# Optimization experiments

Hardware: AMD Instinct MI355X
Metric: run time of the kernel (lower is better)

The kernel has to match this reference:

```python
import jax, jax.numpy as jnp
import numpy as np

B, S, D, H, E = 2, 1024, 1024, 4096, 8


def _xavier(key, shape):
    # matches torch.nn.init.xavier_uniform_ on a 3D tensor: fan_in/out from last two dims
    fan_in, fan_out = shape[-2], shape[-1]
    limit = float(np.sqrt(6.0 / (fan_in + fan_out)))
    return jax.random.uniform(key, shape, jnp.float32, -limit, limit)


def setup_inputs() -> dict:
    key = jax.random.key(0)
    ks = jax.random.split(key, 4)
    x = jax.random.normal(ks[0], (B, S, D), jnp.float32)
    router_w = jax.random.normal(ks[1], (D, E), jnp.float32) * (1.0 / np.sqrt(D))
    router_b = jnp.zeros((E,), jnp.float32)
    fc1_weight = _xavier(ks[2], (E, D, H))
    fc1_bias = jnp.zeros((E, H), jnp.float32)
    fc2_weight = _xavier(ks[3], (E, H, D))
    fc2_bias = jnp.zeros((E, D), jnp.float32)
    return {
        "x": x,
        "router_w": router_w,
        "router_b": router_b,
        "fc1_weight": fc1_weight,
        "fc1_bias": fc1_bias,
        "fc2_weight": fc2_weight,
        "fc2_bias": fc2_bias,
    }


def reference(x, router_w, router_b, fc1_weight, fc1_bias, fc2_weight, fc2_bias):
    b, s, d = x.shape
    x_flat = x.reshape(-1, d)                                  # [T, D]
    logits = x_flat @ router_w + router_b                       # [T, E]
    probs = jax.nn.softmax(logits, axis=-1)                     # [T, E]
    # per-expert FC1 + exact GELU (torch nn.GELU default is erf-based)
    h = jnp.einsum('td,edh->teh', x_flat, fc1_weight) + fc1_bias  # [T, E, H]
    h = jax.nn.gelu(h, approximate=False)
    expert_out = jnp.einsum('teh,ehd->ted', h, fc2_weight) + fc2_bias  # [T, E, D]
    out_flat = jnp.einsum('te,ted->td', probs, expert_out)      # [T, D]
    y = out_flat.reshape(b, s, d)
    router_probs = probs.reshape(b, s, -1)
    return y, router_probs
```

## Files before the change

kernel.cpp:

```cpp
#include <hip/hip_runtime.h>
#include <math.h>


typedef float f32x4 __attribute__((ext_vector_type(4)));
typedef __bf16 bf16x8 __attribute__((ext_vector_type(8)));

#define GLL16(gp, lp)                                                          \
  __builtin_amdgcn_global_load_lds(                                            \
      (const __attribute__((address_space(1))) void*)(gp),                     \
      (__attribute__((address_space(3))) void*)(lp), 16, 0, 0)

__device__ __forceinline__ float gelu_f(float h) {
  float x = h * 0.70710678118654752f;
  float ax = fabsf(x);
  float t = __builtin_amdgcn_rcpf(fmaf(0.3275911f, ax, 1.0f));
  float p = fmaf(1.061405429f, t, -1.453152027f);
  p = fmaf(p, t, 1.421413741f);
  p = fmaf(p, t, -0.284496736f);
  p = fmaf(p, t, 0.254829592f);
  float e = __expf(-x * x);
  float erfv = fmaf(-p * t, e, 1.0f);
  erfv = copysignf(erfv, x);
  return 0.5f * h * (1.0f + erfv);
}

__global__ void pre_kernel(const float* __restrict__ x,
                           const float* __restrict__ rw,
                           const float* __restrict__ rb,
                           const float* __restrict__ b2,
                           float* __restrict__ PT,
                           float* __restrict__ probs_out,
                           __bf16* __restrict__ xb,
                           float* __restrict__ y)
{
  __shared__ float ps[4][8];
  const int tid = threadIdx.x;
  const int g = tid >> 6, l = tid & 63;
  const int t = blockIdx.x * 4 + g;
  const int d0 = l * 16;
  const float* xr = x + (size_t)t * 1024 + d0;

  f32x4 xv[4];
#pragma unroll
  for (int i = 0; i < 4; ++i) xv[i] = *(const f32x4*)(xr + i * 4);

  {
    bf16x8 o0, o1;
#pragma unroll
    for (int j = 0; j < 8; ++j) {
      o0[j] = (__bf16)xv[j >> 2][j & 3];
      o1[j] = (__bf16)xv[2 + (j >> 2)][j & 3];
    }
    *(bf16x8*)(xb + (size_t)t * 1024 + d0) = o0;
    *(bf16x8*)(xb + (size_t)t * 1024 + d0 + 8) = o1;
  }

  float a[8];
#pragma unroll
  for (int e = 0; e < 8; ++e) a[e] = 0.f;
#pragma unroll
  for (int i = 0; i < 16; ++i) {
    float xs = xv[i >> 2][i & 3];
    const float* wr = rw + (size_t)(d0 + i) * 8;
    f32x4 w0 = *(const f32x4*)(wr);
    f32x4 w1 = *(const f32x4*)(wr + 4);
#pragma unroll
    for (int e = 0; e < 4; ++e) a[e] = fmaf(xs, w0[e], a[e]);
#pragma unroll
    for (int e = 0; e < 4; ++e) a[4 + e] = fmaf(xs, w1[e], a[4 + e]);
  }
#pragma unroll
  for (int off = 32; off > 0; off >>= 1) {
#pragma unroll
    for (int e = 0; e < 8; ++e) a[e] += __shfl_down(a[e], off);
  }
  if (l == 0) {
#pragma unroll
    for (int e = 0; e < 8; ++e) a[e] += rb[e];
    float m = a[0];
#pragma unroll
    for (int e = 1; e < 8; ++e) m = fmaxf(m, a[e]);
    float s = 0.f;
#pragma unroll
    for (int e = 0; e < 8; ++e) { a[e] = __expf(a[e] - m); s += a[e]; }
    float inv = 1.f / s;
#pragma unroll
    for (int e = 0; e < 8; ++e) {
      float p = a[e] * inv;
      PT[(size_t)e * 2048 + t] = p;
      probs_out[t * 8 + e] = p;
      ps[g][e] = p;
    }
  }
  __syncthreads();

  f32x4 acc[4];
#pragma unroll
  for (int i = 0; i < 4; ++i) acc[i] = {0.f, 0.f, 0.f, 0.f};
#pragma unroll
  for (int e = 0; e < 8; ++e) {
    float p = ps[g][e];
#pragma unroll
    for (int i = 0; i < 4; ++i) {
      f32x4 b = *(const f32x4*)(b2 + (size_t)e * 1024 + d0 + i * 4);
#pragma unroll
      for (int c = 0; c < 4; ++c) acc[i][c] = fmaf(p, b[c], acc[i][c]);
    }
  }
#pragma unroll
  for (int i = 0; i < 4; ++i)
    *(f32x4*)(y + (size_t)t * 1024 + d0 + i * 4) = acc[i];
}

__global__ void router_kernel(const float* __restrict__ x,
                              const float* __restrict__ rw,
                              const float* __restrict__ rb,
                              float* __restrict__ probs_out)
{
  int gid = blockIdx.x * blockDim.x + threadIdx.x;
  int t = gid >> 6;
  int l = gid & 63;
  const float* xr = x + (size_t)t * 1024;
  float a[8];
#pragma unroll
  for (int e = 0; e < 8; ++e) a[e] = 0.f;
  for (int d = l; d < 1024; d += 64) {
    float xv = xr[d];
    f32x4 w0 = *(const f32x4*)(rw + d * 8);
    f32x4 w1 = *(const f32x4*)(rw + d * 8 + 4);
#pragma unroll
    for (int e = 0; e < 4; ++e) a[e] += xv * w0[e];
#pragma unroll
    for (int e = 0; e < 4; ++e) a[4 + e] += xv * w1[e];
  }
#pragma unroll
  for (int off = 32; off > 0; off >>= 1) {
#pragma unroll
    for (int e = 0; e < 8; ++e) a[e] += __shfl_down(a[e], off);
  }
  if (l == 0) {
#pragma unroll
    for (int e = 0; e < 8; ++e) a[e] += rb[e];
    float m = a[0];
#pragma unroll
    for (int e = 1; e < 8; ++e) m = fmaxf(m, a[e]);
    float s = 0.f;
#pragma unroll
    for (int e = 0; e < 8; ++e) { a[e] = __expf(a[e] - m); s += a[e]; }
    float inv = 1.f / s;
#pragma unroll
    for (int e = 0; e < 8; ++e) probs_out[t * 8 + e] = a[e] * inv;
  }
}

__global__ void transconv_kernel(const float* __restrict__ src,
                                 __bf16* __restrict__ dst,
                                 int R, int C, size_t dstLd, size_t zOff)
{
  __shared__ __bf16 tile[64][257];
  size_t bs = (size_t)blockIdx.z * (size_t)R * (size_t)C;
  size_t dzo = (size_t)blockIdx.z * zOff;
  int r0 = blockIdx.x * 64, c0 = blockIdx.y * 256;
  const int l15 = (threadIdx.x & 15) * 4;
  const int rq = threadIdx.x >> 4;
#pragma unroll
  for (int i = 0; i < 4; ++i) {
    const int row = rq + 16 * i;
    const float* sr = src + bs + (size_t)(r0 + row) * C + c0 + l15;
#pragma unroll
    for (int q = 0; q < 4; ++q) {
      f32x4 v = *(const f32x4*)(sr + q * 64);
#pragma unroll
      for (int j = 0; j < 4; ++j)
        tile[row][q * 64 + l15 + j] = (__bf16)v[j];
    }
  }
  __syncthreads();
  const int cb = threadIdx.x >> 3;
  const int orr = (threadIdx.x & 7) * 8;
#pragma unroll
  for (int g = 0; g < 8; ++g) {
    const int c = cb + 32 * g;
    bf16x8 o;
#pragma unroll
    for (int j = 0; j < 8; ++j) o[j] = tile[orr + j][c];
    *(bf16x8*)(dst + (size_t)(c0 + c) * dstLd + dzo + r0 + orr) = o;
  }
}

__device__ __forceinline__ void mfma_loop256(
    const char* Ab, const char* Bb, size_t ldaB, size_t ldbB, int K,
    char* lds, f32x4 acc[8][4])
{
  const int tid = threadIdx.x;
  const int w = tid >> 6, l = tid & 63;
  const int wm = w >> 2, wn = w & 3;
  const int m16 = l & 15, q = l >> 4;
  const int swz = m16 & 7;
  const int aBase = wm * 16384 + m16 * 128;
  const int bBase = 32768 + (wn >> 1) * 16384 + ((wn & 1) * 64 + m16) * 128;
  const int srcCh = ((l & 7) ^ ((l >> 3) & 7)) << 4;
  const size_t gA0 = (size_t)(w * 16 + (l >> 3)) * ldaB + srcCh;
  const size_t gB0 = (size_t)(w * 16 + (l >> 3)) * ldbB + srcCh;
  const int dstW = w * 2048;
  const int NT = K >> 6;

  bf16x8 af[4][2], bv[4][2];

#define STG_A(h, tau)                                                          \
  {                                                                            \
    char* d = lds + (((tau) & 1) * 65536) + (h) * 16384 + dstW;                \
    const char* g = Ab + gA0 + (size_t)((h) * 128) * ldaB + (size_t)(tau) * 128;\
    GLL16(g, d);                                                               \
    GLL16(g + 8 * ldaB, d + 1024);                                             \
  }
#define STG_B(h, tau)                                                          \
  {                                                                            \
    char* d = lds + (((tau) & 1) * 65536) + 32768 + (h) * 16384 + dstW;        \
    const char* g = Bb + gB0 + (size_t)((h) * 128) * ldbB + (size_t)(tau) * 128;\
    GLL16(g, d);                                                               \
    GLL16(g + 8 * ldbB, d + 1024);                                             \
  }
#define RD_A(lo, p)                                                            \
  _Pragma("unroll") for (int mi = 0; mi < 4; ++mi)                             \
  _Pragma("unroll") for (int ks = 0; ks < 2; ++ks)                             \
    af[mi][ks] = *(const bf16x8*)(lds + (p) * 65536 + aBase +                  \
        ((lo) * 4 + mi) * 2048 + (((ks * 4 + q) ^ swz) << 4));
#define RD_B(no, p)                                                            \
  _Pragma("unroll") for (int nj = 0; nj < 2; ++nj)                             \
  _Pragma("unroll") for (int ks = 0; ks < 2; ++ks)                             \
    bv[(no) * 2 + nj][ks] = *(const bf16x8*)(lds + (p) * 65536 + bBase +       \
        ((no) * 2 + nj) * 2048 + (((ks * 4 + q) ^ swz) << 4));
#define MM(lo, no)                                                             \
  __builtin_amdgcn_s_setprio(1);                                               \
  _Pragma("unroll") for (int mi = 0; mi < 4; ++mi)                             \
  _Pragma("unroll") for (int nj = 0; nj < 2; ++nj)                             \
  _Pragma("unroll") for (int ks = 0; ks < 2; ++ks)                             \
    acc[(lo) * 4 + mi][(no) * 2 + nj] =                                        \
        __builtin_amdgcn_mfma_f32_16x16x32_bf16(                               \
            af[mi][ks], bv[(no) * 2 + nj][ks],                                 \
            acc[(lo) * 4 + mi][(no) * 2 + nj], 0, 0, 0);                       \
  __builtin_amdgcn_s_setprio(0);
#define SB __builtin_amdgcn_sched_barrier(0)
#define BAR { SB; __builtin_amdgcn_s_barrier(); SB; }
#define VMW(n) asm volatile("s_waitcnt vmcnt(" #n ")" ::: "memory")

  STG_A(0, 0); STG_A(1, 0); STG_B(0, 0); STG_B(1, 0);
  STG_B(0, 1); STG_B(1, 1);
  VMW(4);
  BAR;

  int t = 0;
  for (; t < NT - 2; ++t) {
    const int p = t & 1;
    RD_A(0, p); RD_B(0, p);
    STG_A(0, t + 1);
    BAR; MM(0, 0); BAR;
    RD_B(1, p);
    STG_A(1, t + 1);
    BAR; MM(0, 1); BAR;
    RD_A(1, p);
    STG_B(0, t + 2);
    BAR; MM(1, 0); BAR;
    STG_B(1, t + 2);
    BAR; MM(1, 1); SB; VMW(4); BAR;
  }
  {
    const int p = t & 1;
    RD_A(0, p); RD_B(0, p);
    STG_A(0, t + 1);
    BAR; MM(0, 0); BAR;
    RD_B(1, p);
    STG_A(1, t + 1);
    BAR; MM(0, 1); BAR;
    RD_A(1, p);
    BAR; MM(1, 0); BAR;
    BAR; MM(1, 1); SB; VMW(0); BAR;
    ++t;
  }
  {
    const int p = t & 1;
    RD_A(0, p); RD_B(0, p);
    MM(0, 0);
    RD_B(1, p);
    MM(0, 1);
    RD_A(1, p);
    MM(1, 0);
    MM(1, 1);
  }
#undef STG_A
#undef STG_B
#undef RD_A
#undef RD_B
#undef MM
#undef SB
#undef BAR
#undef VMW
}

__device__ __forceinline__ int xcd_swz(int id, int nwg) {
  return ((nwg & 7) == 0) ? ((id & 7) * (nwg >> 3) + (id >> 3)) : id;
}

__global__ __launch_bounds__(512, 2) void gemm1_kernel(
    const __bf16* __restrict__ X, const __bf16* __restrict__ W1T,
    const float* __restrict__ b1, const float* __restrict__ PT,
    __bf16* __restrict__ Hs, int hs_ld, int e_off, size_t b_zstride)
{
  __shared__ __align__(16) char lds[131072];
  const int nwg = gridDim.x * gridDim.y * gridDim.z;
  const int id = blockIdx.x + gridDim.x * (blockIdx.y + gridDim.y * blockIdx.z);
  const int wg = xcd_swz(id, nwg);
  const int bm = wg & 7;
  const int bn = (wg >> 3) % gridDim.y;
  const int z = wg / (gridDim.y << 3);
  const int e = z + e_off;

  f32x4 acc[8][4];
  const f32x4 z4 = {0.f, 0.f, 0.f, 0.f};
#pragma unroll
  for (int i = 0; i < 8; ++i)
#pragma unroll
    for (int j = 0; j < 4; ++j) acc[i][j] = z4;

  const char* A = (const char*)(X + (size_t)bm * 256 * 1024);
  const char* B = (const char*)(W1T + (size_t)z * b_zstride +
                                (size_t)bn * 256 * 1024);
  mfma_loop256(A, B, 2048, 2048, 1024, lds, acc);

  const int tid = threadIdx.x, w = tid >> 6, l = tid & 63;
  const int wm = w >> 2, wn = w & 3, q = l >> 4, m16 = l & 15;
  const int row0 = bm * 256 + wm * 128 + q * 4;
  const int colE = bn * 256 + wn * 64 + m16;
  const int zcol = (hs_ld == 4096) ? 0 : z * 4096;
  float b1v[4];
#pragma unroll
  for (int nj = 0; nj < 4; ++nj)
    b1v[nj] = b1[(size_t)e * 4096 + colE + nj * 16];
#pragma unroll
  for (int mi = 0; mi < 8; ++mi) {
    float pv[4];
#pragma unroll
    for (int r = 0; r < 4; ++r)
      pv[r] = PT[(size_t)e * 2048 + row0 + mi * 16 + r];
#pragma unroll
    for (int nj = 0; nj < 4; ++nj)
#pragma unroll
      for (int r = 0; r < 4; ++r) {
        float h = acc[mi][nj][r] + b1v[nj];
        float o = gelu_f(h) * pv[r];
        Hs[(size_t)(row0 + mi * 16 + r) * hs_ld + zcol + colE + nj * 16] =
            (__bf16)o;
      }
  }
}

__global__ __launch_bounds__(512, 2) void gemm2_kernel(
    const __bf16* __restrict__ Hs, const __bf16* __restrict__ W2T,
    float* __restrict__ y, int lda, int ldb, int kz, int Kb)
{
  __shared__ __align__(16) char lds[131072];
  const int nwg = gridDim.x * gridDim.y * gridDim.z;
  const int id = blockIdx.x + gridDim.x * (blockIdx.y + gridDim.y * blockIdx.z);
  const int wg = xcd_swz(id, nwg);
  const int bm = wg & 7;
  const int bn = (wg >> 3) % gridDim.y;
  const int z = wg / (gridDim.y << 3);

  f32x4 acc[8][4];
  const f32x4 z4 = {0.f, 0.f, 0.f, 0.f};
#pragma unroll
  for (int i = 0; i < 8; ++i)
#pragma unroll
    for (int j = 0; j < 4; ++j) acc[i][j] = z4;

  const char* A = (const char*)(Hs + (size_t)bm * 256 * lda + (size_t)z * kz);
  const char* B = (const char*)(W2T + (size_t)bn * 256 * ldb + (size_t)z * kz);
  mfma_loop256(A, B, (size_t)lda * 2, (size_t)ldb * 2, Kb, lds, acc);

  const int tid = threadIdx.x, w = tid >> 6, l = tid & 63;
  const int wm = w >> 2, wn = w & 3, q = l >> 4, m16 = l & 15;
  const int row0 = bm * 256 + wm * 128 + q * 4;
  const int col0 = bn * 256 + wn * 64 + m16;
#pragma unroll
  for (int mi = 0; mi < 8; ++mi)
#pragma unroll
    for (int nj = 0; nj < 4; ++nj)
#pragma unroll
      for (int r = 0; r < 4; ++r)
        unsafeAtomicAdd(
            y + (size_t)(row0 + mi * 16 + r) * 1024 + col0 + nj * 16,
            acc[mi][nj][r]);
}

__global__ __launch_bounds__(256) void fused_naive_kernel(
    const float* __restrict__ x, const float* __restrict__ w1,
    const float* __restrict__ b1, const float* __restrict__ w2,
    const float* __restrict__ b2, const float* __restrict__ probs,
    float* __restrict__ y)
{
  __shared__ float xs[8][1024];
  __shared__ float gs[8][64];
  __shared__ float ps[8];
  const int tid = threadIdx.x;
  const int t0 = blockIdx.x * 8;
  const size_t DH = (size_t)1024 * 4096;
  const int tt = tid >> 5;
  const int d0 = (tid & 31) * 32;
  float acc[32];
#pragma unroll
  for (int i = 0; i < 32; ++i) acc[i] = 0.f;
  {
    const f32x4* xsrc = (const f32x4*)(x + (size_t)t0 * 1024);
    f32x4* xdst = (f32x4*)&xs[0][0];
    for (int i = tid; i < 2048; i += 256) xdst[i] = xsrc[i];
  }
  const int wv = tid >> 6;
  const int hl = tid & 63;
  for (int e = 0; e < 8; ++e) {
    if (tid < 8) ps[tid] = probs[(size_t)(t0 + tid) * 8 + e];
    __syncthreads();
    for (int hc = 0; hc < 4096; hc += 64) {
      float a0 = 0.f, a1 = 0.f;
      const float* w1p = w1 + (size_t)e * DH + hc + hl;
      for (int d = 0; d < 1024; ++d) {
        float wvv = w1p[(size_t)d * 4096];
        a0 += xs[wv * 2 + 0][d] * wvv;
        a1 += xs[wv * 2 + 1][d] * wvv;
      }
      __syncthreads();
      gs[wv * 2 + 0][hl] =
          ps[wv * 2 + 0] * gelu_f(a0 + b1[(size_t)e * 4096 + hc + hl]);
      gs[wv * 2 + 1][hl] =
          ps[wv * 2 + 1] * gelu_f(a1 + b1[(size_t)e * 4096 + hc + hl]);
      __syncthreads();
      const float* w2p = w2 + (size_t)e * DH + (size_t)hc * 1024 + d0;
      for (int hh = 0; hh < 64; ++hh) {
        float g = gs[tt][hh];
#pragma unroll
        for (int jb = 0; jb < 8; ++jb) {
          f32x4 w4 = *(const f32x4*)(w2p + (size_t)hh * 1024 + jb * 4);
#pragma unroll
          for (int j2 = 0; j2 < 4; ++j2) acc[jb * 4 + j2] += g * w4[j2];
        }
      }
    }
#pragma unroll
    for (int j = 0; j < 32; ++j)
      acc[j] += ps[tt] * b2[(size_t)e * 1024 + d0 + j];
    __syncthreads();
  }
  float* yp = y + (size_t)(t0 + tt) * 1024 + d0;
#pragma unroll
  for (int jb = 0; jb < 8; ++jb) {
    f32x4 o = {acc[jb * 4], acc[jb * 4 + 1], acc[jb * 4 + 2], acc[jb * 4 + 3]};
    *(f32x4*)(yp + jb * 4) = o;
  }
}

extern "C" void kernel_launch(void* const* d_in, const int* in_sizes, int n_in,
                              void* d_out, int out_size, void* d_ws,
                              size_t ws_size, hipStream_t stream)
{
  const float* x  = (const float*)d_in[0];
  const float* rw = (const float*)d_in[1];
  const float* rb = (const float*)d_in[2];
  const float* w1 = (const float*)d_in[3];
  const float* b1 = (const float*)d_in[4];
  const float* w2 = (const float*)d_in[5];
  const float* b2 = (const float*)d_in[6];
  float* y = (float*)d_out;
  float* probs_out = y + (size_t)2048 * 1024;

  const size_t DH = (size_t)1024 * 4096;
  const size_t BASE = (64 << 10) + (size_t)2048 * 1024 * 2;
  const size_t TA = BASE + 8 * DH * 2 + (size_t)2048 * 32768 * 2;
  const size_t TB = BASE + DH * 2 + (size_t)2048 * 4096 * 2;

  char* ws = (char*)d_ws;
  float* PT = (float*)ws;
  __bf16* xb = (__bf16*)(ws + (64 << 10));
  __bf16* WT = (__bf16*)(ws + BASE);

  if (ws_size >= TA) {
    pre_kernel<<<512, 256, 0, stream>>>(x, rw, rb, b2, PT, probs_out, xb, y);
    __bf16* Hs = WT + 8 * DH;
    transconv_kernel<<<dim3(16, 16, 8), 256, 0, stream>>>(
        w1, WT, 1024, 4096, 1024, DH);
    gemm1_kernel<<<dim3(8, 16, 8), 512, 0, stream>>>(xb, WT, b1, PT, Hs,
                                                     32768, 0, DH);
    transconv_kernel<<<dim3(64, 4, 8), 256, 0, stream>>>(
        w2, WT, 4096, 1024, 32768, 4096);
    gemm2_kernel<<<dim3(8, 4, 8), 512, 0, stream>>>(Hs, WT, y, 32768,
                                                    32768, 4096, 4096);
  } else if (ws_size >= TB) {
    pre_kernel<<<512, 256, 0, stream>>>(x, rw, rb, b2, PT, probs_out, xb, y);
    __bf16* HsE = WT + DH;
    for (int e = 0; e < 8; ++e) {
      transconv_kernel<<<dim3(16, 16, 1), 256, 0, stream>>>(
          w1 + (size_t)e * DH, WT, 1024, 4096, 1024, 0);
      gemm1_kernel<<<dim3(8, 16, 1), 512, 0, stream>>>(xb, WT, b1, PT, HsE,
                                                       4096, e, 0);
      transconv_kernel<<<dim3(64, 4, 1), 256, 0, stream>>>(
          w2 + (size_t)e * DH, WT, 4096, 1024, 4096, 0);
      gemm2_kernel<<<dim3(8, 4, 4), 512, 0, stream>>>(HsE, WT, y, 4096,
                                                      4096, 1024, 1024);
    }
  } else {
    router_kernel<<<512, 256, 0, stream>>>(x, rw, rb, probs_out);
    fused_naive_kernel<<<256, 256, 0, stream>>>(x, w1, b1, w2, b2, probs_out,
                                                y);
  }
}
```

Measured before the change: 607.6 us.

## Restructure MFMA main loop into two half-phases with fewer barriers

Reorganizes the double-buffered bf16 MFMA K-loop so each tile iteration issues all B and half of A LDS reads up front, runs two larger MFMA groups, and uses two workgroup barriers instead of eight. Sched_barrier fences are removed so the compiler can interleave LDS reads, global-to-LDS loads and MFMAs more freely, and the setprio window now spans a whole half-tile. The transpose-convert kernel is split into two named kernels for separate profiling. The risk is more live fragment registers and possible LDS hazards if the compiler reorders loads across the fewer barriers.

```diff
diff --git a/kernel.cpp b/kernel.cpp
--- a/kernel.cpp
+++ b/kernel.cpp
@@ -153,9 +153,10 @@
   }
 }
 
-__global__ void transconv_kernel(const float* __restrict__ src,
-                                 __bf16* __restrict__ dst,
-                                 int R, int C, size_t dstLd, size_t zOff)
+__device__ __forceinline__ void transconv_body(const float* __restrict__ src,
+                                               __bf16* __restrict__ dst,
+                                               int R, int C, size_t dstLd,
+                                               size_t zOff)
 {
   __shared__ __bf16 tile[64][257];
   size_t bs = (size_t)blockIdx.z * (size_t)R * (size_t)C;
@@ -187,6 +188,16 @@
     *(bf16x8*)(dst + (size_t)(c0 + c) * dstLd + dzo + r0 + orr) = o;
   }
 }
+
+__global__ void transconv1_kernel(const float* __restrict__ src,
+                                  __bf16* __restrict__ dst,
+                                  int R, int C, size_t dstLd, size_t zOff)
+{ transconv_body(src, dst, R, C, dstLd, zOff); }
+
+__global__ void transconv2_kernel(const float* __restrict__ src,
+                                  __bf16* __restrict__ dst,
+                                  int R, int C, size_t dstLd, size_t zOff)
+{ transconv_body(src, dst, R, C, dstLd, zOff); }
 
 __device__ __forceinline__ void mfma_loop256(
     const char* Ab, const char* Bb, size_t ldaB, size_t ldbB, int K,
@@ -232,69 +243,64 @@
     bv[(no) * 2 + nj][ks] = *(const bf16x8*)(lds + (p) * 65536 + bBase +       \
         ((no) * 2 + nj) * 2048 + (((ks * 4 + q) ^ swz) << 4));
 #define MM(lo, no)                                                             \
-  __builtin_amdgcn_s_setprio(1);                                               \
   _Pragma("unroll") for (int mi = 0; mi < 4; ++mi)                             \
   _Pragma("unroll") for (int nj = 0; nj < 2; ++nj)                             \
   _Pragma("unroll") for (int ks = 0; ks < 2; ++ks)                             \
     acc[(lo) * 4 + mi][(no) * 2 + nj] =                                        \
         __builtin_amdgcn_mfma_f32_16x16x32_bf16(                               \
             af[mi][ks], bv[(no) * 2 + nj][ks],                                 \
-            acc[(lo) * 4 + mi][(no) * 2 + nj], 0, 0, 0);                       \
+            acc[(lo) * 4 + mi][(no) * 2 + nj], 0, 0, 0);
+#define MMP(lo)                                                                \
+  __builtin_amdgcn_s_setprio(1);                                               \
+  MM(lo, 0); MM(lo, 1);                                                        \
   __builtin_amdgcn_s_setprio(0);
-#define SB __builtin_amdgcn_sched_barrier(0)
-#define BAR { SB; __builtin_amdgcn_s_barrier(); SB; }
+#define BARR __builtin_amdgcn_s_barrier()
 #define VMW(n) asm volatile("s_waitcnt vmcnt(" #n ")" ::: "memory")
 
   STG_A(0, 0); STG_A(1, 0); STG_B(0, 0); STG_B(1, 0);
   STG_B(0, 1); STG_B(1, 1);
   VMW(4);
-  BAR;
+  BARR;
 
   int t = 0;
   for (; t < NT - 2; ++t) {
     const int p = t & 1;
-    RD_A(0, p); RD_B(0, p);
-    STG_A(0, t + 1);
-    BAR; MM(0, 0); BAR;
-    RD_B(1, p);
-    STG_A(1, t + 1);
-    BAR; MM(0, 1); BAR;
+    RD_B(0, p); RD_B(1, p); RD_A(0, p);
+    STG_A(0, t + 1); STG_A(1, t + 1);
+    MMP(0);
+    BARR;
+    STG_B(0, t + 2); STG_B(1, t + 2);
     RD_A(1, p);
-    STG_B(0, t + 2);
-    BAR; MM(1, 0); BAR;
-    STG_B(1, t + 2);
-    BAR; MM(1, 1); SB; VMW(4); BAR;
+    MMP(1);
+    VMW(4);
+    BARR;
   }
   {
     const int p = t & 1;
-    RD_A(0, p); RD_B(0, p);
-    STG_A(0, t + 1);
-    BAR; MM(0, 0); BAR;
-    RD_B(1, p);
-    STG_A(1, t + 1);
-    BAR; MM(0, 1); BAR;
+    RD_B(0, p); RD_B(1, p); RD_A(0, p);
+    STG_A(0, t + 1); STG_A(1, t + 1);
+    MMP(0);
+    BARR;
     RD_A(1, p);
-    BAR; MM(1, 0); BAR;
-    BAR; MM(1, 1); SB; VMW(0); BAR;
+    MMP(1);
+    VMW(0);
+    BARR;
     ++t;
   }
   {
     const int p = t & 1;
-    RD_A(0, p); RD_B(0, p);
-    MM(0, 0);
-    RD_B(1, p);
-    MM(0, 1);
+    RD_B(0, p); RD_B(1, p); RD_A(0, p);
+    MMP(0);
     RD_A(1, p);
-    MM(1, 0);
-    MM(1, 1);
+    MMP(1);
   }
 #undef STG_A
 #undef STG_B
 #undef RD_A
 #undef RD_B
 #undef MM
-#undef SB
-#undef BAR
+#undef MMP
+#undef BARR
 #undef VMW
 }
 
@@ -485,11 +491,11 @@
   if (ws_size >= TA) {
     pre_kernel<<<512, 256, 0, stream>>>(x, rw, rb, b2, PT, probs_out, xb, y);
     __bf16* Hs = WT + 8 * DH;
-    transconv_kernel<<<dim3(16, 16, 8), 256, 0, stream>>>(
+    transconv1_kernel<<<dim3(16, 16, 8), 256, 0, stream>>>(
         w1, WT, 1024, 4096, 1024, DH);
     gemm1_kernel<<<dim3(8, 16, 8), 512, 0, stream>>>(xb, WT, b1, PT, Hs,
                                                      32768, 0, DH);
-    transconv_kernel<<<dim3(64, 4, 8), 256, 0, stream>>>(
+    transconv2_kernel<<<dim3(64, 4, 8), 256, 0, stream>>>(
         w2, WT, 4096, 1024, 32768, 4096);
     gemm2_kernel<<<dim3(8, 4, 8), 512, 0, stream>>>(Hs, WT, y, 32768,
                                                     32768, 4096, 4096);
@@ -497,11 +503,11 @@
     pre_kernel<<<512, 256, 0, stream>>>(x, rw, rb, b2, PT, probs_out, xb, y);
     __bf16* HsE = WT + DH;
     for (int e = 0; e < 8; ++e) {
-      transconv_kernel<<<dim3(16, 16, 1), 256, 0, stream>>>(
+      transconv1_kernel<<<dim3(16, 16, 1), 256, 0, stream>>>(
           w1 + (size_t)e * DH, WT, 1024, 4096, 1024, 0);
       gemm1_kernel<<<dim3(8, 16, 1), 512, 0, stream>>>(xb, WT, b1, PT, HsE,
                                                        4096, e, 0);
-      transconv_kernel<<<dim3(64, 4, 1), 256, 0, stream>>>(
+      transconv2_kernel<<<dim3(64, 4, 1), 256, 0, stream>>>(
           w2 + (size_t)e * DH, WT, 4096, 1024, 4096, 0);
       gemm2_kernel<<<dim3(8, 4, 4), 512, 0, stream>>>(HsE, WT, y, 4096,
                                                       4096, 1024, 1024);
```

Result: no change. 609.8 us (+0.4%).

## Rework weight transpose-convert tiling and store W2T per-expert contiguous

Applied to the files above, without the earlier changes.

The fp32-to-bf16 transpose kernel now uses tall tiles (up to 2048 rows by 32 columns) that are transposed as they are written to LDS, so each output row is emitted as long contiguous bf16x8 runs. The W2 transpose also changes layout from one wide interleaved matrix (ld 32768) to a contiguous block per expert (ld 4096, offset DH), and gemm2 takes a separate per-expert B offset to match. The aim is more coalesced, longer writes and a more compact B operand for gemm2. The cost is far fewer blocks per transpose launch and a large LDS tile, which lowers occupancy, plus column-strided LDS writes that may bank-conflict.

```diff
diff --git a/kernel.cpp b/kernel.cpp
--- a/kernel.cpp
+++ b/kernel.cpp
@@ -155,36 +155,41 @@
 
 __global__ void transconv_kernel(const float* __restrict__ src,
                                  __bf16* __restrict__ dst,
-                                 int R, int C, size_t dstLd, size_t zOff)
-{
-  __shared__ __bf16 tile[64][257];
-  size_t bs = (size_t)blockIdx.z * (size_t)R * (size_t)C;
-  size_t dzo = (size_t)blockIdx.z * zOff;
-  int r0 = blockIdx.x * 64, c0 = blockIdx.y * 256;
-  const int l15 = (threadIdx.x & 15) * 4;
-  const int rq = threadIdx.x >> 4;
-#pragma unroll
-  for (int i = 0; i < 4; ++i) {
-    const int row = rq + 16 * i;
-    const float* sr = src + bs + (size_t)(r0 + row) * C + c0 + l15;
-#pragma unroll
-    for (int q = 0; q < 4; ++q) {
-      f32x4 v = *(const f32x4*)(sr + q * 64);
+                                 int R, int C, int RB,
+                                 size_t dstLd, size_t zOff)
+{
+  __shared__ __bf16 tile[32][2056];
+  const size_t bs = (size_t)blockIdx.z * (size_t)R * (size_t)C;
+  const size_t dzo = (size_t)blockIdx.z * zOff;
+  const int r0 = blockIdx.x * RB, c0 = blockIdx.y * 32;
+  const int tid = threadIdx.x;
+
+  {
+    const int lc = tid & 7, rg = tid >> 3;
+    const int ni = RB >> 5;
+    for (int i = 0; i < ni; ++i) {
+      const int r = rg + 32 * i;
+      f32x4 v = *(const f32x4*)(src + bs + (size_t)(r0 + r) * C + c0 + lc * 4);
 #pragma unroll
       for (int j = 0; j < 4; ++j)
-        tile[row][q * 64 + l15 + j] = (__bf16)v[j];
+        tile[lc * 4 + j][r] = (__bf16)v[j];
     }
   }
   __syncthreads();
-  const int cb = threadIdx.x >> 3;
-  const int orr = (threadIdx.x & 7) * 8;
-#pragma unroll
-  for (int g = 0; g < 8; ++g) {
-    const int c = cb + 32 * g;
-    bf16x8 o;
-#pragma unroll
-    for (int j = 0; j < 8; ++j) o[j] = tile[orr + j][c];
-    *(bf16x8*)(dst + (size_t)(c0 + c) * dstLd + dzo + r0 + orr) = o;
+
+  {
+    const int oc = tid >> 4, ol = tid & 15;
+    const int ns = RB >> 7;
+#pragma unroll
+    for (int co = 0; co < 2; ++co) {
+      const int c = oc + 16 * co;
+      __bf16* dcol = dst + (size_t)(c0 + c) * dstLd + dzo + r0;
+      for (int s = 0; s < ns; ++s) {
+        const int rr = ol * 8 + s * 128;
+        bf16x8 o = *(const bf16x8*)(&tile[c][rr]);
+        *(bf16x8*)(dcol + rr) = o;
+      }
+    }
   }
 }
 
@@ -357,7 +362,7 @@
 
 __global__ __launch_bounds__(512, 2) void gemm2_kernel(
     const __bf16* __restrict__ Hs, const __bf16* __restrict__ W2T,
-    float* __restrict__ y, int lda, int ldb, int kz, int Kb)
+    float* __restrict__ y, int lda, int ldb, int akz, size_t bzoff, int Kb)
 {
   __shared__ __align__(16) char lds[131072];
   const int nwg = gridDim.x * gridDim.y * gridDim.z;
@@ -374,8 +379,9 @@
 #pragma unroll
     for (int j = 0; j < 4; ++j) acc[i][j] = z4;
 
-  const char* A = (const char*)(Hs + (size_t)bm * 256 * lda + (size_t)z * kz);
-  const char* B = (const char*)(W2T + (size_t)bn * 256 * ldb + (size_t)z * kz);
+  const char* A = (const char*)(Hs + (size_t)bm * 256 * lda + (size_t)z * akz);
+  const char* B = (const char*)(W2T + (size_t)z * bzoff +
+                                (size_t)bn * 256 * ldb);
   mfma_loop256(A, B, (size_t)lda * 2, (size_t)ldb * 2, Kb, lds, acc);
 
   const int tid = threadIdx.x, w = tid >> 6, l = tid & 63;
@@ -485,26 +491,26 @@
   if (ws_size >= TA) {
     pre_kernel<<<512, 256, 0, stream>>>(x, rw, rb, b2, PT, probs_out, xb, y);
     __bf16* Hs = WT + 8 * DH;
-    transconv_kernel<<<dim3(16, 16, 8), 256, 0, stream>>>(
-        w1, WT, 1024, 4096, 1024, DH);
+    transconv_kernel<<<dim3(1, 128, 8), 256, 0, stream>>>(
+        w1, WT, 1024, 4096, 1024, 1024, DH);
     gemm1_kernel<<<dim3(8, 16, 8), 512, 0, stream>>>(xb, WT, b1, PT, Hs,
                                                      32768, 0, DH);
-    transconv_kernel<<<dim3(64, 4, 8), 256, 0, stream>>>(
-        w2, WT, 4096, 1024, 32768, 4096);
+    transconv_kernel<<<dim3(2, 32, 8), 256, 0, stream>>>(
+        w2, WT, 4096, 1024, 2048, 4096, DH);
     gemm2_kernel<<<dim3(8, 4, 8), 512, 0, stream>>>(Hs, WT, y, 32768,
-                                                    32768, 4096, 4096);
+                                                    4096, 4096, DH, 4096);
   } else if (ws_size >= TB) {
     pre_kernel<<<512, 256, 0, stream>>>(x, rw, rb, b2, PT, probs_out, xb, y);
     __bf16* HsE = WT + DH;
     for (int e = 0; e < 8; ++e) {
-      transconv_kernel<<<dim3(16, 16, 1), 256, 0, stream>>>(
-          w1 + (size_t)e * DH, WT, 1024, 4096, 1024, 0);
+      transconv_kernel<<<dim3(1, 128, 1), 256, 0, stream>>>(
+          w1 + (size_t)e * DH, WT, 1024, 4096, 1024, 1024, 0);
       gemm1_kernel<<<dim3(8, 16, 1), 512, 0, stream>>>(xb, WT, b1, PT, HsE,
                                                        4096, e, 0);
-      transconv_kernel<<<dim3(64, 4, 1), 256, 0, stream>>>(
-          w2 + (size_t)e * DH, WT, 4096, 1024, 4096, 0);
-      gemm2_kernel<<<dim3(8, 4, 4), 512, 0, stream>>>(HsE, WT, y, 4096,
-                                                      4096, 1024, 1024);
+      transconv_kernel<<<dim3(2, 32, 1), 256, 0, stream>>>(
+          w2 + (size_t)e * DH, WT, 4096, 1024, 2048, 4096, 0);
+      gemm2_kernel<<<dim3(8, 4, 4), 512, 0, stream>>>(
+          HsE, WT, y, 4096, 4096, 1024, 1024, 1024);
     }
   } else {
     router_kernel<<<512, 256, 0, stream>>>(x, rw, rb, probs_out);
```

New measurement: 614.8 us. Within noise of the previous version (+1.2%).
